# Kernel optimization log

Hardware: AMD Instinct MI355X
Metric: run time of the kernel (lower is better)

## Reference

```python
import jax, jax.numpy as jnp
import numpy as np
import math

CHI, CHO, UP = 256, 128, 2
KH = KW = 3


def bilinear_up_kernel(k):
    f = math.ceil(k / 2)
    c = (2 * f - 1 - f % 2) / (2.0 * f)
    w = np.zeros((k, k), dtype=np.float32)
    for i in range(k):
        for j in range(k):
            w[i, j] = (1 - abs(i / f - c)) * (1 - abs(j / f - c))
    return w


def setup_inputs() -> dict:
    key = jax.random.key(0)
    ks = jax.random.split(key, 8)
    x = jax.random.normal(ks[0], (8, CHI, 64, 64), dtype=jnp.float32)
    # DCNv2 weights
    w_dcn = jax.random.normal(ks[1], (CHO, CHI, KH, KW), dtype=jnp.float32) * 0.02
    b_dcn = jnp.zeros((CHO,), dtype=jnp.float32)
    # offset/mask conv: out channels = 3*KH*KW (2*9 offsets + 9 mask), zero-init as in DCNv2
    w_off = jnp.zeros((3 * KH * KW, CHI, KH, KW), dtype=jnp.float32)
    b_off = jnp.zeros((3 * KH * KW,), dtype=jnp.float32)
    # BatchNorm (eval math) params
    bn_gamma = jax.random.uniform(ks[2], (CHO,), dtype=jnp.float32, minval=0.5, maxval=1.5)
    bn_beta = jax.random.normal(ks[3], (CHO,), dtype=jnp.float32) * 0.1
    bn_mean = jax.random.normal(ks[4], (CHO,), dtype=jnp.float32) * 0.1
    bn_var = jax.random.uniform(ks[5], (CHO,), dtype=jnp.float32, minval=0.5, maxval=1.5)
    # fixed bilinear depthwise transpose-conv weights [CHO,1,2r,2r]
    w_up = jnp.broadcast_to(jnp.asarray(bilinear_up_kernel(UP * 2)), (CHO, 1, UP * 2, UP * 2)).astype(jnp.float32)
    # 1x1 conv to 1 channel
    w_1x1 = jax.random.normal(ks[6], (1, CHO, 1, 1), dtype=jnp.float32) * 0.05
    return dict(x=x, w_dcn=w_dcn, b_dcn=b_dcn, w_off=w_off, b_off=b_off,
                bn_gamma=bn_gamma, bn_beta=bn_beta, bn_mean=bn_mean, bn_var=bn_var,
                w_up=w_up, w_1x1=w_1x1)


def conv2d(x, w, b=None, stride=1, pad=1):
    y = jax.lax.conv_general_dilated(x, w, (stride, stride), [(pad, pad), (pad, pad)],
                                     dimension_numbers=('NCHW', 'OIHW', 'NCHW'))
    if b is not None:
        y = y + b[None, :, None, None]
    return y


def bilinear_sample(img, py, px):
    # img: [C,H,W]; py,px: [P] float coords. Zero padding outside.
    C, H, W = img.shape
    y0 = jnp.floor(py); x0 = jnp.floor(px)
    y1 = y0 + 1; x1 = x0 + 1
    wy1 = py - y0; wy0 = 1.0 - wy1
    wx1 = px - x0; wx0 = 1.0 - wx1

    def gather(yi, xi):
        valid = (yi >= 0) & (yi < H) & (xi >= 0) & (xi < W)
        yc = jnp.clip(yi, 0, H - 1).astype(jnp.int32)
        xc = jnp.clip(xi, 0, W - 1).astype(jnp.int32)
        v = img[:, yc, xc]  # [C,P]
        return v * valid.astype(img.dtype)[None, :]

    out = (gather(y0, x0) * (wy0 * wx0)[None, :] + gather(y0, x1) * (wy0 * wx1)[None, :]
           + gather(y1, x0) * (wy1 * wx0)[None, :] + gather(y1, x1) * (wy1 * wx1)[None, :])
    return out  # [C,P]


def dcn_v2(x, w, b, offset, mask):
    # x: [B,Ci,H,W]; offset: [B,2*K,H,W]; mask: [B,K,H,W]; K=9; stride 1, pad 1.
    B, Ci, H, W = x.shape
    K = KH * KW
    # base sampling grid per kernel tap
    ky, kx = jnp.meshgrid(jnp.arange(KH) - 1, jnp.arange(KW) - 1, indexing='ij')  # [3,3]
    oy, ox = jnp.meshgrid(jnp.arange(H), jnp.arange(W), indexing='ij')  # [H,W]
    base_y = oy[None, :, :] + ky.reshape(K, 1, 1)  # [K,H,W]
    base_x = ox[None, :, :] + kx.reshape(K, 1, 1)

    off = offset.reshape(B, K, 2, H, W)
    py = base_y[None] + off[:, :, 0]  # [B,K,H,W]
    px = base_x[None] + off[:, :, 1]

    def per_sample(img, py_b, px_b, m_b):
        samp = bilinear_sample(img, py_b.reshape(-1), px_b.reshape(-1))  # [Ci, K*H*W]
        samp = samp.reshape(Ci, K, H, W) * m_b[None]  # [Ci,K,H,W]
        # conv accumulate: w [Co,Ci,KH,KW] -> [Co,Ci,K]
        return jnp.einsum('cik,ikhw->chw', w.reshape(w.shape[0], Ci, K), samp[None].swapaxes(0, 1).squeeze(1)[None].squeeze(0)[None].squeeze(0).reshape(Ci, K, H, W))

    def per_sample2(img, py_b, px_b, m_b):
        samp = bilinear_sample(img, py_b.reshape(-1), px_b.reshape(-1)).reshape(Ci, K, H, W)
        samp = samp * m_b[None]
        return jnp.einsum('oik,ikhw->ohw', w.reshape(w.shape[0], Ci, K), samp)

    y = jax.vmap(per_sample2)(x, py, px, mask)  # [B,Co,H,W]
    return y + b[None, :, None, None]


def reference(x, w_dcn, b_dcn, w_off, b_off, bn_gamma, bn_beta, bn_mean, bn_var, w_up, w_1x1):
    K = KH * KW
    om = conv2d(x, w_off, b_off, stride=1, pad=1)  # [B,3K,H,W]
    o1, o2, m = om[:, :K], om[:, K:2 * K], om[:, 2 * K:]
    # DCNv2 ordering: offsets interleaved as (dy,dx) per tap -> o1=dy, o2=dx
    offset = jnp.concatenate([o1[:, :, None], o2[:, :, None]], axis=2).reshape(x.shape[0], 2 * K, x.shape[2], x.shape[3])
    mask = jax.nn.sigmoid(m)
    y = dcn_v2(x, w_dcn, b_dcn, offset, mask)
    # BN (eval) + ReLU
    inv = jax.lax.rsqrt(bn_var + 1e-5)
    y = jax.nn.relu((y - bn_mean[None, :, None, None]) * (bn_gamma * inv)[None, :, None, None] + bn_beta[None, :, None, None])
    # depthwise transpose conv, kernel 2r, stride r, pad r//2
    r = UP
    y = jax.lax.conv_transpose(y, w_up.transpose(2, 3, 1, 0),  # HWIO with I=1 (feature_group_count)
                               strides=(r, r), padding=[(r // 2, r // 2), (r // 2, r // 2)],
                               dimension_numbers=('NCHW', 'HWIO', 'NCHW'),
                               transpose_kernel=True)
    # NOTE: jax.lax.conv_transpose lacks groups; emulate depthwise via per-channel trick below instead.
    return y


def depthwise_conv_transpose(y, w_up, r):
    # y: [B,C,H,W]; w_up: [C,1,k,k]; equivalent to input-dilated conv with flipped kernel
    C = y.shape[1]
    k = w_up.shape[2]
    wf = w_up[:, :, ::-1, ::-1]  # flip for transpose conv
    pad = k - 1 - r // 2
    return jax.lax.conv_general_dilated(y, wf, window_strides=(1, 1),
                                        padding=[(pad, pad), (pad, pad)],
                                        lhs_dilation=(r, r),
                                        dimension_numbers=('NCHW', 'OIHW', 'NCHW'),
                                        feature_group_count=C)


def reference(x, w_dcn, b_dcn, w_off, b_off, bn_gamma, bn_beta, bn_mean, bn_var, w_up, w_1x1):
    K = KH * KW
    om = conv2d(x, w_off, b_off, stride=1, pad=1)
    o1, o2, m = om[:, :K], om[:, K:2 * K], om[:, 2 * K:]
    offset = jnp.concatenate([o1[:, :, None], o2[:, :, None]], axis=2).reshape(x.shape[0], 2 * K, x.shape[2], x.shape[3])
    mask = jax.nn.sigmoid(m)
    y = dcn_v2(x, w_dcn, b_dcn, offset, mask)
    inv = jax.lax.rsqrt(bn_var + 1e-5)
    y = jax.nn.relu((y - bn_mean[None, :, None, None]) * (bn_gamma * inv)[None, :, None, None] + bn_beta[None, :, None, None])
    y = depthwise_conv_transpose(y, w_up, UP)  # [B,CHO,2H,2W]
    y = conv2d(y, w_1x1, None, stride=1, pad=0)  # [B,1,2H,2W]
    return jax.nn.sigmoid(y)
```

## Files before the change

### kernel.cpp

```cpp
#include <hip/hip_runtime.h>
#include <math.h>

typedef __attribute__((ext_vector_type(8))) short short8;
typedef __attribute__((ext_vector_type(4))) float floatx4;

__device__ __forceinline__ unsigned short bf16r(float f) {
  union { float f; unsigned int u; } v; v.f = f;
  unsigned int u = v.u;
  return (unsigned short)((u + 0x7fffu + ((u >> 16) & 1u)) >> 16);
}
__device__ __forceinline__ unsigned int bf16h(float f) {
  union { float f; unsigned int u; } v; v.f = f;
  return (v.u + 0x8000u) >> 16;
}
__device__ __forceinline__ float bf2f(unsigned int u) {
  union { unsigned int u; float f; } v; v.u = u << 16; return v.f;
}
__device__ __forceinline__ void glds16(const void* g, void* l) {
  __builtin_amdgcn_global_load_lds(
      (const __attribute__((address_space(1))) unsigned int*)g,
      (__attribute__((address_space(3))) unsigned int*)l, 16, 0, 0);
}

__global__ __launch_bounds__(256) void k_pre(
    const float* __restrict__ x,
    const float* __restrict__ w_dcn, const float* __restrict__ w_off,
    const float* __restrict__ b_dcn,
    const float* __restrict__ bn_g, const float* __restrict__ bn_b,
    const float* __restrict__ bn_m, const float* __restrict__ bn_v,
    const float* __restrict__ w_up, const float* __restrict__ w1x1,
    unsigned short* __restrict__ xT,
    unsigned short* __restrict__ wt_dcn, unsigned short* __restrict__ wt_off,
    float* __restrict__ vtab, float* __restrict__ bntab,
    unsigned int* __restrict__ offflags) {
  __shared__ unsigned short sx[32 * 264];
  int e = blockIdx.x * 256 + threadIdx.x;
  if (e < 294912) {
    int s = e >> 12;
    int r = e & 4095;
    int ot = r >> 9;
    int lane = (r >> 3) & 63;
    int j = e & 7;
    int l15 = lane & 15, quad = lane >> 4;
    int o = ot * 16 + l15;
    int k = s % 9, cg = s / 9;
    int c = cg * 32 + quad * 8 + j;
    wt_dcn[e] = bf16r(w_dcn[(o * 256 + c) * 9 + k]);
  }
  bool nz = false;
  if (e < 73728) {
    int cg = e / 9216;
    int r = e % 9216;
    int frag = r >> 9;
    int k = frag >> 1, ot = frag & 1;
    int lane = (r >> 3) & 63, j = e & 7;
    int l15 = lane & 15, quad = lane >> 4;
    int oc = ot * 16 + l15;
    int c = cg * 32 + quad * 8 + j;
    float wv = (oc < 27) ? w_off[(oc * 256 + c) * 9 + k] : 0.f;
    wt_off[e] = bf16r(wv);
    nz = (wv != 0.f);
  }
  unsigned long long ba = __ballot(nz);
  if (blockIdx.x < 288 && (threadIdx.x & 63) == 0)
    offflags[blockIdx.x * 4 + (threadIdx.x >> 6)] = (ba != 0ull) ? 1u : 0u;
  if (e < 2048) {
    int o = e >> 4;
    vtab[e] = w1x1[o] * w_up[e];
  }
  if (e < 128) {
    float g = bn_g[e] * rsqrtf(bn_v[e] + 1e-5f);
    bntab[e] = g;
    bntab[128 + e] = (b_dcn[e] - bn_m[e]) * g + bn_b[e];
  }
  if (blockIdx.x < 1024) {
    int b = blockIdx.x & 7, px0 = ((blockIdx.x >> 3) & 127) * 32;
    int t = threadIdx.x;
    int px = t & 31, cg = t >> 5;
    const float* xsrc = x + (((size_t)(b * 256 + cg * 32)) << 12) + px0 + px;
#pragma unroll
    for (int cc = 0; cc < 32; ++cc)
      sx[px * 264 + cg * 32 + cc] = bf16r(xsrc[(size_t)cc << 12]);
    __syncthreads();
#pragma unroll
    for (int j = 0; j < 4; ++j) {
      int unit = t + j * 256;
      int p = unit >> 5, chunk = unit & 31;
      uint4 v = *(const uint4*)&sx[p * 264 + chunk * 8];
      *(uint4*)&xT[((size_t)((b << 12) + px0 + p)) * 256 + chunk * 8] = v;
    }
  }
}

__global__ __launch_bounds__(256, 3) void k_dcnu(
    const unsigned short* __restrict__ xT, const unsigned short* __restrict__ wt,
    const float* __restrict__ b_off, const float* __restrict__ vtab,
    const float* __restrict__ bntab, const unsigned int* __restrict__ offflags,
    float* __restrict__ R) {
  int b = blockIdx.x & 7, row = blockIdx.x >> 3;
  __shared__ unsigned short sW[2 * 12288];
  __shared__ unsigned int s_fl[8];
  int t = threadIdx.x, lane = t & 63, wvx = t >> 6;
  int l15 = lane & 15, quad = lane >> 4;
  int px = wvx * 16 + l15;
  const unsigned short* xb = xT + (((size_t)b) << 12) * 256;
  const short8 zz = {0, 0, 0, 0, 0, 0, 0, 0};

  {
    unsigned int a = 0;
    for (int i = t; i < 1152; i += 256) a |= offflags[i];
    unsigned int bo = (lane < 27 && b_off[lane] != 0.f) ? 1u : 0u;
    a = __any(a != 0u) ? 1u : 0u;
    bo = __any(bo != 0u) ? 1u : 0u;
    if (lane == 0) { s_fl[wvx] = a; s_fl[4 + wvx] = bo; }
  }
  __syncthreads();
  if ((s_fl[0] | s_fl[1] | s_fl[2] | s_fl[3] |
       s_fl[4] | s_fl[5] | s_fl[6] | s_fl[7]) != 0u)
    return;

  {
    int wr0 = max(row - 1, 0), wr1 = min(row + 1, 63);
    for (int rr = wr0; rr <= wr1; ++rr) {
      const uint4* src = (const uint4*)(xb + ((size_t)(rr << 6)) * 256);
#pragma unroll
      for (int i = 0; i < 8; ++i) {
        uint4 v = src[t + (i << 8)];
        asm volatile("" :: "v"(v.x), "v"(v.y), "v"(v.z), "v"(v.w));
      }
    }
  }

  int pixk[9]; bool vkk[9];
#pragma unroll
  for (int k = 0; k < 9; ++k) {
    int yy = row + k / 3 - 1, xx = px + k % 3 - 1;
    vkk[k] = ((unsigned)yy < 64u) & ((unsigned)xx < 64u);
    pixk[k] = vkk[k] ? (yy * 64 + xx) : 0;
  }

  floatx4 acc[8];
#pragma unroll
  for (int i = 0; i < 8; ++i) acc[i] = (floatx4){0.f, 0.f, 0.f, 0.f};

  uint4 traw[3];
  {
    int cbase = quad * 8;
#pragma unroll
    for (int kk = 0; kk < 3; ++kk)
      traw[kk] = *(const uint4*)&xb[(size_t)pixk[kk] * 256 + cbase];
  }
  {
#pragma unroll
    for (int i = 0; i < 6; ++i) {
      int blk = wvx * 6 + i;
      glds16(wt + (size_t)blk * 512 + lane * 8, &sW[blk * 512]);
    }
  }
  __syncthreads();

  for (int phase = 0; phase < 24; ++phase) {
    unsigned short* buf = sW + (phase & 1) * 12288;
    unsigned short* nbuf = sW + ((phase + 1) & 1) * 12288;
    if (phase < 23) {
      const unsigned short* wsrc = wt + (size_t)(phase + 1) * 12288;
#pragma unroll
      for (int i = 0; i < 6; ++i) {
        int blk = wvx * 6 + i;
        glds16(wsrc + (size_t)blk * 512 + lane * 8, &nbuf[blk * 512]);
      }
    }
    int nphase = phase + 1;
    int ncbase = (nphase / 3) * 32 + quad * 8;

#pragma unroll
    for (int kk = 0; kk < 3; ++kk) {
      int k = (phase % 3) * 3 + kk;
      union { uint4 u; short8 s; } bx; bx.u = traw[kk];
      short8 bs = vkk[k] ? bx.s : zz;
      if (phase < 23) {
        int nk = (nphase % 3) * 3 + kk;
        traw[kk] = *(const uint4*)&xb[(size_t)pixk[nk] * 256 + ncbase];
      }
      const unsigned short* bk = buf + kk * 4096 + lane * 8;
#pragma unroll
      for (int ot = 0; ot < 8; ++ot) {
        short8 af = *(const short8*)&bk[ot * 512];
        acc[ot] = __builtin_amdgcn_mfma_f32_16x16x32_bf16(af, bs, acc[ot], 0, 0, 0);
      }
    }
    __syncthreads();
  }

  float* sv = (float*)sW;
  float* sbn = sv + 2176;
  for (int i = t; i < 2048; i += 256) sv[(i >> 4) * 17 + (i & 15)] = vtab[i];
  if (t < 256) sbn[t] = bntab[t];
  __syncthreads();

  float rpart[16];
#pragma unroll
  for (int i = 0; i < 16; ++i) rpart[i] = 0.f;
#pragma unroll
  for (int ot = 0; ot < 8; ++ot)
#pragma unroll
    for (int r = 0; r < 4; ++r) {
      int o = ot * 16 + quad * 4 + r;
      float yv = fmaxf(acc[ot][r] * (0.5f * sbn[o]) + sbn[128 + o], 0.f);
      const float* vp = &sv[o * 17];
#pragma unroll
      for (int tt = 0; tt < 16; ++tt) rpart[tt] += vp[tt] * yv;
    }
#pragma unroll
  for (int tt = 0; tt < 16; ++tt) {
    rpart[tt] += __shfl_xor(rpart[tt], 16, 64);
    rpart[tt] += __shfl_xor(rpart[tt], 32, 64);
  }
#pragma unroll
  for (int j = 0; j < 4; ++j) {
    int slot = quad * 4 + j;
    R[(((size_t)(b * 16 + slot)) << 12) + row * 64 + px] = rpart[slot];
  }
}

__global__ __launch_bounds__(256, 2) void k_dcng(
    const unsigned short* __restrict__ xT, const unsigned short* __restrict__ wt,
    const unsigned short* __restrict__ wtoff, const float* __restrict__ b_off,
    const float* __restrict__ vtab, const float* __restrict__ bntab,
    const unsigned int* __restrict__ offflags, float* __restrict__ R) {
  int b = blockIdx.x & 7, row = blockIdx.x >> 3;
  __shared__ unsigned short sW[2 * 12288];
  __shared__ ushort4 s_ti[576];
  __shared__ float4 s_tw[576];
  __shared__ unsigned int s_fl[8];
  int t = threadIdx.x, lane = t & 63, wvx = t >> 6;
  int l15 = lane & 15, quad = lane >> 4;
  int px = wvx * 16 + l15;
  const unsigned short* xb = xT + (((size_t)b) << 12) * 256;
  const short8 zz = {0, 0, 0, 0, 0, 0, 0, 0};
  unsigned short* som = (unsigned short*)s_ti;

  {
    unsigned int a = 0;
    for (int i = t; i < 1152; i += 256) a |= offflags[i];
    unsigned int bo = (lane < 27 && b_off[lane] != 0.f) ? 1u : 0u;
    a = __any(a != 0u) ? 1u : 0u;
    bo = __any(bo != 0u) ? 1u : 0u;
    if (lane == 0) { s_fl[wvx] = a; s_fl[4 + wvx] = bo; }
  }
  __syncthreads();
  const bool offnz = (s_fl[0] | s_fl[1] | s_fl[2] | s_fl[3]) != 0u;
  const bool bofnz = (s_fl[4] | s_fl[5] | s_fl[6] | s_fl[7]) != 0u;
  if (!offnz && !bofnz) return;

  if (!offnz) {
    int wr0 = max(row - 1, 0), wr1 = min(row + 1, 63);
    for (int rr = wr0; rr <= wr1; ++rr) {
      const uint4* src = (const uint4*)(xb + ((size_t)(rr << 6)) * 256);
#pragma unroll
      for (int i = 0; i < 8; ++i) {
        uint4 v = src[t + (i << 8)];
        asm volatile("" :: "v"(v.x), "v"(v.y), "v"(v.z), "v"(v.w));
      }
    }
  }

  if (offnz) {
    int pixk[9]; bool vkk[9];
#pragma unroll
    for (int k = 0; k < 9; ++k) {
      int yy = row + k / 3 - 1, xx = px + k % 3 - 1;
      vkk[k] = ((unsigned)yy < 64u) & ((unsigned)xx < 64u);
      pixk[k] = vkk[k] ? (yy * 64 + xx) : 0;
    }
    floatx4 oacc[2];
    oacc[0] = (floatx4){0.f, 0.f, 0.f, 0.f};
    oacc[1] = (floatx4){0.f, 0.f, 0.f, 0.f};

#pragma unroll
    for (int i = 0; i < 5; ++i) {
      int frag = wvx + i * 4;
      if (frag < 18)
        glds16(wtoff + (size_t)frag * 512 + lane * 8, &sW[frag * 512]);
    }
    __syncthreads();

    for (int cg = 0; cg < 8; ++cg) {
      unsigned short* buf = sW + (cg & 1) * 9216;
      int cb = cg * 32 + quad * 8;
      short8 bx[9];
#pragma unroll
      for (int k = 0; k < 9; ++k) {
        short8 v = *(const short8*)&xb[(size_t)pixk[k] * 256 + cb];
        bx[k] = vkk[k] ? v : zz;
      }
      if (cg < 7) {
        const unsigned short* wsrc = wtoff + (size_t)(cg + 1) * 9216;
        unsigned short* nbuf = sW + ((cg + 1) & 1) * 9216;
#pragma unroll
        for (int i = 0; i < 5; ++i) {
          int frag = wvx + i * 4;
          if (frag < 18)
            glds16(wsrc + (size_t)frag * 512 + lane * 8, &nbuf[frag * 512]);
        }
      }
#pragma unroll
      for (int k = 0; k < 9; ++k) {
        short8 a0 = *(const short8*)&buf[(k * 2 + 0) * 512 + lane * 8];
        short8 a1 = *(const short8*)&buf[(k * 2 + 1) * 512 + lane * 8];
        oacc[0] = __builtin_amdgcn_mfma_f32_16x16x32_bf16(a0, bx[k], oacc[0], 0, 0, 0);
        oacc[1] = __builtin_amdgcn_mfma_f32_16x16x32_bf16(a1, bx[k], oacc[1], 0, 0, 0);
      }
      __syncthreads();
    }
#pragma unroll
    for (int ot = 0; ot < 2; ++ot)
#pragma unroll
      for (int r = 0; r < 4; ++r) {
        int o = ot * 16 + quad * 4 + r;
        if (o < 27) som[o * 64 + px] = bf16r(oacc[ot][r] + b_off[o]);
      }
    __syncthreads();
  }

  {
    float to1[3], to2[3], tmv[3];
    if (offnz) {
#pragma unroll
      for (int ii = 0; ii < 3; ++ii) {
        int i = t + ii * 256;
        if (i < 576) {
          int k = i >> 6, p = i & 63;
          to1[ii] = bf2f(som[k * 64 + p]);
          to2[ii] = bf2f(som[(9 + k) * 64 + p]);
          tmv[ii] = bf2f(som[(18 + k) * 64 + p]);
        }
      }
      __syncthreads();
    } else {
#pragma unroll
      for (int ii = 0; ii < 3; ++ii) {
        int i = t + ii * 256;
        if (i < 576) {
          int k = i >> 6;
          to1[ii] = bf2f(bf16r(b_off[k]));
          to2[ii] = bf2f(bf16r(b_off[9 + k]));
          tmv[ii] = bf2f(bf16r(b_off[18 + k]));
        }
      }
    }
#pragma unroll
    for (int ii = 0; ii < 3; ++ii) {
      int i = t + ii * 256;
      if (i < 576) {
        int k = i >> 6, p = i & 63;
        float m = 1.f / (1.f + __expf(-tmv[ii]));
        float py = (float)(row + k / 3 - 1) + to1[ii];
        float pxf = (float)(p + (k % 3) - 1) + to2[ii];
        float fy = floorf(py), fx = floorf(pxf);
        int iy = (int)fy, ix = (int)fx;
        float wy1 = py - fy, wy0 = 1.f - wy1;
        float wx1 = pxf - fx, wx0 = 1.f - wx1;
        bool y0ok = (iy >= 0) & (iy < 64), y1ok = (iy >= -1) & (iy < 63);
        bool x0ok = (ix >= 0) & (ix < 64), x1ok = (ix >= -1) & (ix < 63);
        int iy0 = min(max(iy, 0), 63), iy1 = min(max(iy + 1, 0), 63);
        int ix0 = min(max(ix, 0), 63), ix1 = min(max(ix + 1, 0), 63);
        s_ti[i] = make_ushort4((unsigned short)(iy0 * 64 + ix0), (unsigned short)(iy0 * 64 + ix1),
                               (unsigned short)(iy1 * 64 + ix0), (unsigned short)(iy1 * 64 + ix1));
        float4 w;
        w.x = (y0ok && x0ok) ? m * wy0 * wx0 : 0.f;
        w.y = (y0ok && x1ok) ? m * wy0 * wx1 : 0.f;
        w.z = (y1ok && x0ok) ? m * wy1 * wx0 : 0.f;
        w.w = (y1ok && x1ok) ? m * wy1 * wx1 : 0.f;
        s_tw[i] = w;
      }
    }
  }
  __syncthreads();

  const uint4 z4 = make_uint4(0u, 0u, 0u, 0u);

  floatx4 acc[8];
#pragma unroll
  for (int i = 0; i < 8; ++i) acc[i] = (floatx4){0.f, 0.f, 0.f, 0.f};

  uint4 traw[12];
  {
    int cbase = quad * 8;
#pragma unroll
    for (int kk = 0; kk < 3; ++kk) {
      ushort4 ti = s_ti[(kk << 6) + px];
      float4 twn = s_tw[(kk << 6) + px];
      uint4 t0 = z4, t1 = z4, t2 = z4, t3 = z4;
      if (__any(twn.x != 0.f)) t0 = *(const uint4*)&xb[(size_t)ti.x * 256 + cbase];
      if (__any(twn.y != 0.f)) t1 = *(const uint4*)&xb[(size_t)ti.y * 256 + cbase];
      if (__any(twn.z != 0.f)) t2 = *(const uint4*)&xb[(size_t)ti.z * 256 + cbase];
      if (__any(twn.w != 0.f)) t3 = *(const uint4*)&xb[(size_t)ti.w * 256 + cbase];
      traw[kk * 4 + 0] = t0; traw[kk * 4 + 1] = t1;
      traw[kk * 4 + 2] = t2; traw[kk * 4 + 3] = t3;
    }
  }
  {
    const unsigned short* wsrc = wt;
#pragma unroll
    for (int i = 0; i < 6; ++i) {
      int blk = wvx * 6 + i;
      glds16(wsrc + (size_t)blk * 512 + lane * 8, &sW[blk * 512]);
    }
  }
  __syncthreads();

  int lofs = lane * 8;

  for (int phase = 0; phase < 24; ++phase) {
    unsigned short* buf = sW + (phase & 1) * 12288;
    unsigned short* nbuf = sW + ((phase + 1) & 1) * 12288;
    if (phase < 23) {
      const unsigned short* wsrc = wt + (size_t)(phase + 1) * 12288;
#pragma unroll
      for (int i = 0; i < 6; ++i) {
        int blk = wvx * 6 + i;
        glds16(wsrc + (size_t)blk * 512 + lane * 8, &nbuf[blk * 512]);
      }
    }
    int nphase = phase + 1;
    int ncbase = (nphase / 3) * 32 + quad * 8;

#pragma unroll
    for (int kk = 0; kk < 3; ++kk) {
      int k = (phase % 3) * 3 + kk;
      float4 tw = s_tw[(k << 6) + px];
      union { uint4 u; short8 s; } x0, x1, x2, x3;
      x0.u = traw[kk * 4 + 0]; x1.u = traw[kk * 4 + 1];
      x2.u = traw[kk * 4 + 2]; x3.u = traw[kk * 4 + 3];
      if (phase < 23) {
        int nk = (nphase % 3) * 3 + kk;
        ushort4 ti = s_ti[(nk << 6) + px];
        float4 twn = s_tw[(nk << 6) + px];
        uint4 t0 = z4, t1 = z4, t2 = z4, t3 = z4;
        if (__any(twn.x != 0.f)) t0 = *(const uint4*)&xb[(size_t)ti.x * 256 + ncbase];
        if (__any(twn.y != 0.f)) t1 = *(const uint4*)&xb[(size_t)ti.y * 256 + ncbase];
        if (__any(twn.z != 0.f)) t2 = *(const uint4*)&xb[(size_t)ti.z * 256 + ncbase];
        if (__any(twn.w != 0.f)) t3 = *(const uint4*)&xb[(size_t)ti.w * 256 + ncbase];
        traw[kk * 4 + 0] = t0; traw[kk * 4 + 1] = t1;
        traw[kk * 4 + 2] = t2; traw[kk * 4 + 3] = t3;
      }
      float r[8];
#pragma unroll
      for (int j = 0; j < 8; ++j) r[j] = tw.x * bf2f((unsigned short)x0.s[j]);
      if (__any(tw.y != 0.f)) {
#pragma unroll
        for (int j = 0; j < 8; ++j) r[j] += tw.y * bf2f((unsigned short)x1.s[j]);
      }
      if (__any(tw.z != 0.f)) {
#pragma unroll
        for (int j = 0; j < 8; ++j) r[j] += tw.z * bf2f((unsigned short)x2.s[j]);
      }
      if (__any(tw.w != 0.f)) {
#pragma unroll
        for (int j = 0; j < 8; ++j) r[j] += tw.w * bf2f((unsigned short)x3.s[j]);
      }
      union { uint4 u; short8 s; } bu;
      bu.u = make_uint4(bf16h(r[0]) | (bf16h(r[1]) << 16), bf16h(r[2]) | (bf16h(r[3]) << 16),
                        bf16h(r[4]) | (bf16h(r[5]) << 16), bf16h(r[6]) | (bf16h(r[7]) << 16));
      const unsigned short* bk = buf + kk * 4096 + lofs;
#pragma unroll
      for (int ot = 0; ot < 8; ++ot) {
        short8 af = *(const short8*)&bk[ot * 512];
        acc[ot] = __builtin_amdgcn_mfma_f32_16x16x32_bf16(af, bu.s, acc[ot], 0, 0, 0);
      }
    }
    __syncthreads();
  }

  float* sv = (float*)sW;
  float* sbn = sv + 2176;
  for (int i = t; i < 2048; i += 256) sv[(i >> 4) * 17 + (i & 15)] = vtab[i];
  if (t < 256) sbn[t] = bntab[t];
  __syncthreads();

  float rpart[16];
#pragma unroll
  for (int i = 0; i < 16; ++i) rpart[i] = 0.f;
#pragma unroll
  for (int ot = 0; ot < 8; ++ot)
#pragma unroll
    for (int r = 0; r < 4; ++r) {
      int o = ot * 16 + quad * 4 + r;
      float yv = fmaxf(acc[ot][r] * sbn[o] + sbn[128 + o], 0.f);
      const float* vp = &sv[o * 17];
#pragma unroll
      for (int tt = 0; tt < 16; ++tt) rpart[tt] += vp[tt] * yv;
    }
#pragma unroll
  for (int tt = 0; tt < 16; ++tt) {
    rpart[tt] += __shfl_xor(rpart[tt], 16, 64);
    rpart[tt] += __shfl_xor(rpart[tt], 32, 64);
  }
#pragma unroll
  for (int j = 0; j < 4; ++j) {
    int slot = quad * 4 + j;
    R[(((size_t)(b * 16 + slot)) << 12) + row * 64 + px] = rpart[slot];
  }
}

__global__ __launch_bounds__(256) void k_upb(
    const float* __restrict__ R, float* __restrict__ out) {
  int b = blockIdx.x & 7, sub = blockIdx.x >> 3;
  int inner = sub * 256 + threadIdx.x;
  int X = inner & 127, Y = inner >> 7;
  int i0, wu0, wu1, j0, wv0, wv1;
  if (Y & 1) { i0 = (Y - 1) >> 1; wu0 = 2; wu1 = 0; }
  else       { i0 = (Y - 2) / 2;  wu0 = 3; wu1 = 1; }
  if (X & 1) { j0 = (X - 1) >> 1; wv0 = 2; wv1 = 0; }
  else       { j0 = (X - 2) / 2;  wv0 = 3; wv1 = 1; }
  int i1 = i0 + 1, j1 = j0 + 1;
  float mi0 = ((unsigned)i0 < 64u) ? 1.f : 0.f;
  float mi1 = ((unsigned)i1 < 64u) ? 1.f : 0.f;
  float mj0 = ((unsigned)j0 < 64u) ? 1.f : 0.f;
  float mj1 = ((unsigned)j1 < 64u) ? 1.f : 0.f;
  int i0c = min(max(i0, 0), 63), i1c = min(max(i1, 0), 63);
  int j0c = min(max(j0, 0), 63), j1c = min(max(j1, 0), 63);
  const float* Rb = R + (((size_t)b) << 16);
  float s = mi0 * mj0 * Rb[((wu0 * 4 + wv0) << 12) + (i0c << 6) + j0c] +
            mi0 * mj1 * Rb[((wu0 * 4 + wv1) << 12) + (i0c << 6) + j1c] +
            mi1 * mj0 * Rb[((wu1 * 4 + wv0) << 12) + (i1c << 6) + j0c] +
            mi1 * mj1 * Rb[((wu1 * 4 + wv1) << 12) + (i1c << 6) + j1c];
  out[(b << 14) + inner] = 1.f / (1.f + __expf(-s));
}

extern "C" void kernel_launch(void* const* d_in, const int* in_sizes, int n_in,
                              void* d_out, int out_size, void* d_ws, size_t ws_size,
                              hipStream_t stream) {
  const float* x        = (const float*)d_in[0];
  const float* w_dcn    = (const float*)d_in[1];
  const float* b_dcn    = (const float*)d_in[2];
  const float* w_off    = (const float*)d_in[3];
  const float* b_off    = (const float*)d_in[4];
  const float* bn_gamma = (const float*)d_in[5];
  const float* bn_beta  = (const float*)d_in[6];
  const float* bn_mean  = (const float*)d_in[7];
  const float* bn_var   = (const float*)d_in[8];
  const float* w_up     = (const float*)d_in[9];
  const float* w_1x1    = (const float*)d_in[10];
  float* out = (float*)d_out;

  float* ws = (float*)d_ws;
  unsigned short* xT     = (unsigned short*)ws;
  unsigned short* wt_dcn = (unsigned short*)(ws + 4194304);
  unsigned short* wt_off = (unsigned short*)(ws + 4341760);
  float* vtab            = ws + 4378624;
  float* bntab           = ws + 4380672;
  unsigned int* offflags = (unsigned int*)(ws + 4380928);
  float* R               = ws + 4823296;

  k_pre<<<1152, 256, 0, stream>>>(x, w_dcn, w_off, b_dcn, bn_gamma, bn_beta,
                                  bn_mean, bn_var, w_up, w_1x1,
                                  xT, wt_dcn, wt_off, vtab, bntab, offflags);
  k_dcnu<<<512, 256, 0, stream>>>(xT, wt_dcn, b_off, vtab, bntab, offflags, R);
  k_dcng<<<512, 256, 0, stream>>>(xT, wt_dcn, wt_off, b_off, vtab, bntab,
                                  offflags, R);
  k_upb<<<512, 256, 0, stream>>>(R, out);
}
```

Measured before the change: 143.9 us.

## Stage input rows in LDS and split waves over output-channel/pixel tiles

The unmasked DCN path now stages each needed input row slice in shared memory through async global-to-LDS loads with double buffering. The three horizontal taps then read B fragments from LDS instead of issuing per-lane global gathers. Work is repartitioned so each wave handles half the output channels for two 16-pixel groups, which reuses each A fragment across two MFMAs, and partial sums from the two channel halves are combined through an LDS reduction. This adds LDS usage and extra barriers, and lowers the occupancy hint from 3 to 2 blocks per CU.

```diff
diff --git a/kernel.cpp b/kernel.cpp
--- a/kernel.cpp
+++ b/kernel.cpp
@@ -92,17 +92,20 @@
   }
 }
 
-__global__ __launch_bounds__(256, 3) void k_dcnu(
+__global__ __launch_bounds__(256, 2) void k_dcnu(
     const unsigned short* __restrict__ xT, const unsigned short* __restrict__ wt,
     const float* __restrict__ b_off, const float* __restrict__ vtab,
     const float* __restrict__ bntab, const unsigned int* __restrict__ offflags,
     float* __restrict__ R) {
   int b = blockIdx.x & 7, row = blockIdx.x >> 3;
   __shared__ unsigned short sW[2 * 12288];
+  __shared__ unsigned short sB[2 * 2048];
+  __shared__ float sred[64 * 17];
   __shared__ unsigned int s_fl[8];
   int t = threadIdx.x, lane = t & 63, wvx = t >> 6;
   int l15 = lane & 15, quad = lane >> 4;
-  int px = wvx * 16 + l15;
+  int oh = wvx >> 1;
+  int ph = wvx & 1;
   const unsigned short* xb = xT + (((size_t)b) << 12) * 256;
   const short8 zz = {0, 0, 0, 0, 0, 0, 0, 0};
 
@@ -119,74 +122,64 @@
        s_fl[4] | s_fl[5] | s_fl[6] | s_fl[7]) != 0u)
     return;
 
+  floatx4 acc[4][2];
+#pragma unroll
+  for (int i = 0; i < 4; ++i)
+#pragma unroll
+    for (int j = 0; j < 2; ++j) acc[i][j] = (floatx4){0.f, 0.f, 0.f, 0.f};
+
+#pragma unroll
+  for (int i = 0; i < 6; ++i) {
+    int blk = wvx * 6 + i;
+    glds16(wt + (size_t)blk * 512 + lane * 8, &sW[blk * 512]);
+  }
   {
-    int wr0 = max(row - 1, 0), wr1 = min(row + 1, 63);
-    for (int rr = wr0; rr <= wr1; ++rr) {
-      const uint4* src = (const uint4*)(xb + ((size_t)(rr << 6)) * 256);
-#pragma unroll
-      for (int i = 0; i < 8; ++i) {
-        uint4 v = src[t + (i << 8)];
-        asm volatile("" :: "v"(v.x), "v"(v.y), "v"(v.z), "v"(v.w));
-      }
-    }
-  }
-
-  int pixk[9]; bool vkk[9];
-#pragma unroll
-  for (int k = 0; k < 9; ++k) {
-    int yy = row + k / 3 - 1, xx = px + k % 3 - 1;
-    vkk[k] = ((unsigned)yy < 64u) & ((unsigned)xx < 64u);
-    pixk[k] = vkk[k] ? (yy * 64 + xx) : 0;
-  }
-
-  floatx4 acc[8];
-#pragma unroll
-  for (int i = 0; i < 8; ++i) acc[i] = (floatx4){0.f, 0.f, 0.f, 0.f};
-
-  uint4 traw[3];
-  {
-    int cbase = quad * 8;
-#pragma unroll
-    for (int kk = 0; kk < 3; ++kk)
-      traw[kk] = *(const uint4*)&xb[(size_t)pixk[kk] * 256 + cbase];
-  }
-  {
-#pragma unroll
-    for (int i = 0; i < 6; ++i) {
-      int blk = wvx * 6 + i;
-      glds16(wt + (size_t)blk * 512 + lane * 8, &sW[blk * 512]);
-    }
+    int rowk = row - 1;
+    if (rowk >= 0)
+      glds16(xb + (size_t)(rowk * 64 + wvx * 16 + (lane >> 2)) * 256 + (lane & 3) * 8,
+             &sB[wvx * 512]);
   }
   __syncthreads();
 
   for (int phase = 0; phase < 24; ++phase) {
-    unsigned short* buf = sW + (phase & 1) * 12288;
-    unsigned short* nbuf = sW + ((phase + 1) & 1) * 12288;
+    const unsigned short* bufW = sW + (phase & 1) * 12288;
+    const unsigned short* bufB = sB + (phase & 1) * 2048;
     if (phase < 23) {
-      const unsigned short* wsrc = wt + (size_t)(phase + 1) * 12288;
+      int np = phase + 1;
+      unsigned short* nW = sW + (np & 1) * 12288;
+      const unsigned short* wsrc = wt + (size_t)np * 12288;
 #pragma unroll
       for (int i = 0; i < 6; ++i) {
         int blk = wvx * 6 + i;
-        glds16(wsrc + (size_t)blk * 512 + lane * 8, &nbuf[blk * 512]);
-      }
-    }
-    int nphase = phase + 1;
-    int ncbase = (nphase / 3) * 32 + quad * 8;
-
-#pragma unroll
-    for (int kk = 0; kk < 3; ++kk) {
-      int k = (phase % 3) * 3 + kk;
-      union { uint4 u; short8 s; } bx; bx.u = traw[kk];
-      short8 bs = vkk[k] ? bx.s : zz;
-      if (phase < 23) {
-        int nk = (nphase % 3) * 3 + kk;
-        traw[kk] = *(const uint4*)&xb[(size_t)pixk[nk] * 256 + ncbase];
-      }
-      const unsigned short* bk = buf + kk * 4096 + lane * 8;
-#pragma unroll
-      for (int ot = 0; ot < 8; ++ot) {
-        short8 af = *(const short8*)&bk[ot * 512];
-        acc[ot] = __builtin_amdgcn_mfma_f32_16x16x32_bf16(af, bs, acc[ot], 0, 0, 0);
+        glds16(wsrc + (size_t)blk * 512 + lane * 8, &nW[blk * 512]);
+      }
+      int rowk_n = row + np % 3 - 1;
+      if ((unsigned)rowk_n < 64u)
+        glds16(xb + (size_t)(rowk_n * 64 + wvx * 16 + (lane >> 2)) * 256 +
+                   (np / 3) * 32 + (lane & 3) * 8,
+               &sB[((np & 1) * 2048) + wvx * 512]);
+    }
+    int rowk = row + phase % 3 - 1;
+    if ((unsigned)rowk < 64u) {
+#pragma unroll
+      for (int kx = 0; kx < 3; ++kx) {
+        short8 bf[2];
+#pragma unroll
+        for (int pg = 0; pg < 2; ++pg) {
+          int pxe = (ph * 2 + pg) * 16 + l15 + kx - 1;
+          bool v = (unsigned)pxe < 64u;
+          int pxc = min(max(pxe, 0), 63);
+          union { uint4 u; short8 s; } bb;
+          bb.u = *(const uint4*)&bufB[pxc * 32 + quad * 8];
+          bf[pg] = v ? bb.s : zz;
+        }
+        const unsigned short* ak = bufW + kx * 4096 + (oh * 4) * 512 + lane * 8;
+#pragma unroll
+        for (int oi = 0; oi < 4; ++oi) {
+          short8 af = *(const short8*)&ak[oi * 512];
+          acc[oi][0] = __builtin_amdgcn_mfma_f32_16x16x32_bf16(af, bf[0], acc[oi][0], 0, 0, 0);
+          acc[oi][1] = __builtin_amdgcn_mfma_f32_16x16x32_bf16(af, bf[1], acc[oi][1], 0, 0, 0);
+        }
       }
     }
     __syncthreads();
@@ -198,28 +191,53 @@
   if (t < 256) sbn[t] = bntab[t];
   __syncthreads();
 
-  float rpart[16];
-#pragma unroll
-  for (int i = 0; i < 16; ++i) rpart[i] = 0.f;
-#pragma unroll
-  for (int ot = 0; ot < 8; ++ot)
+  float rpart[2][16];
+#pragma unroll
+  for (int pg = 0; pg < 2; ++pg)
+#pragma unroll
+    for (int i = 0; i < 16; ++i) rpart[pg][i] = 0.f;
+#pragma unroll
+  for (int oi = 0; oi < 4; ++oi)
 #pragma unroll
     for (int r = 0; r < 4; ++r) {
-      int o = ot * 16 + quad * 4 + r;
-      float yv = fmaxf(acc[ot][r] * (0.5f * sbn[o]) + sbn[128 + o], 0.f);
+      int o = (oh * 4 + oi) * 16 + quad * 4 + r;
+      float g = 0.5f * sbn[o], bta = sbn[128 + o];
       const float* vp = &sv[o * 17];
 #pragma unroll
-      for (int tt = 0; tt < 16; ++tt) rpart[tt] += vp[tt] * yv;
-    }
-#pragma unroll
-  for (int tt = 0; tt < 16; ++tt) {
-    rpart[tt] += __shfl_xor(rpart[tt], 16, 64);
-    rpart[tt] += __shfl_xor(rpart[tt], 32, 64);
-  }
+      for (int pg = 0; pg < 2; ++pg) {
+        float yv = fmaxf(acc[oi][pg][r] * g + bta, 0.f);
+#pragma unroll
+        for (int tt = 0; tt < 16; ++tt) rpart[pg][tt] += vp[tt] * yv;
+      }
+    }
+#pragma unroll
+  for (int pg = 0; pg < 2; ++pg)
+#pragma unroll
+    for (int tt = 0; tt < 16; ++tt) {
+      rpart[pg][tt] += __shfl_xor(rpart[pg][tt], 16, 64);
+      rpart[pg][tt] += __shfl_xor(rpart[pg][tt], 32, 64);
+    }
+  if (oh == 0 && lane < 16) {
+#pragma unroll
+    for (int pg = 0; pg < 2; ++pg)
+#pragma unroll
+      for (int tt = 0; tt < 16; ++tt)
+        sred[((ph * 2 + pg) * 16 + lane) * 17 + tt] = rpart[pg][tt];
+  }
+  __syncthreads();
+  if (oh == 1 && lane < 16) {
+#pragma unroll
+    for (int pg = 0; pg < 2; ++pg)
+#pragma unroll
+      for (int tt = 0; tt < 16; ++tt)
+        sred[((ph * 2 + pg) * 16 + lane) * 17 + tt] += rpart[pg][tt];
+  }
+  __syncthreads();
 #pragma unroll
   for (int j = 0; j < 4; ++j) {
-    int slot = quad * 4 + j;
-    R[(((size_t)(b * 16 + slot)) << 12) + row * 64 + px] = rpart[slot];
+    int idx = t + j * 256;
+    int slot = idx >> 6, pxs = idx & 63;
+    R[(((size_t)(b * 16 + slot)) << 12) + row * 64 + pxs] = sred[pxs * 17 + slot];
   }
 }
 
```

Measured after the change: 128.1 us. -11.0%, faster.
